# Kernel tuning notes

Measured on AMD Instinct MI355X. Metric: run time of the kernel, lower is better.

## Reference

```python
import jax, jax.numpy as jnp
import numpy as np
import math

SEQ_LEN = 2048
EMB = 1024
HEAD = 64
BATCH = 8

def setup_inputs() -> dict:
    key = jax.random.key(0)
    k1, k2, k3, k4 = jax.random.split(key, 4)
    x = jax.random.normal(k1, (BATCH, SEQ_LEN, EMB), dtype=jnp.float32)
    # torch Linear(no bias): out = x @ W.T with W [out,in]; store as [in,out]
    s = 1.0 / math.sqrt(EMB)
    Wk = jax.random.uniform(k2, (EMB, HEAD), dtype=jnp.float32, minval=-s, maxval=s)
    Wq = jax.random.uniform(k3, (EMB, HEAD), dtype=jnp.float32, minval=-s, maxval=s)
    Wv = jax.random.uniform(k4, (EMB, HEAD), dtype=jnp.float32, minval=-s, maxval=s)
    return {"x": x, "Wk": Wk, "Wq": Wq, "Wv": Wv}

def reference(x, Wk, Wq, Wv):
    B, S, E = x.shape
    H = Wk.shape[1]
    k = x @ Wk  # [B,S,H]
    q = x @ Wq
    v = x @ Wv
    scores = jnp.einsum('bsh,bth->bst', q, k) / math.sqrt(H)
    causal = jnp.tril(jnp.ones((S, S), dtype=bool))
    scores = jnp.where(causal[None], scores, -jnp.inf)
    attn = jax.nn.softmax(scores, axis=-1)
    # dropout is identity in eval mode
    return jnp.einsum('bst,bth->bsh', attn, v)
```

## Files before the change

kernel.cpp:

```cpp
#include <hip/hip_runtime.h>
#include <hip/hip_bf16.h>

typedef __attribute__((ext_vector_type(8))) short short8;
typedef __attribute__((ext_vector_type(4))) short short4v;
typedef __attribute__((ext_vector_type(4))) float floatx4;

#define SEQ   2048
#define EMB   1024
#define HEAD  64
#define BATCH 8

__device__ __forceinline__ short f2bf(float f) {
    union { float f; unsigned u; } a; a.f = f;
    unsigned u = a.u;
    u = (u + 0x7FFFu + ((u >> 16) & 1u)) >> 16;
    return (short)u;
}

__global__ void wtrans_kernel(const float* __restrict__ Wk,
                              const float* __restrict__ Wq,
                              const float* __restrict__ Wv,
                              short* __restrict__ Wf) {
    int gid  = blockIdx.x * 256 + threadIdx.x;
    int lane = gid & 63;
    int fid  = gid >> 6;
    int chunk = fid & 31;
    int mnt  = fid >> 5;
    int mat  = mnt >> 2, nt = mnt & 3;
    const float* src = (mat == 0) ? Wq : (mat == 1) ? Wk : Wv;
    int n = lane & 15, quad = lane >> 4;
    int h = nt * 16 + n;
    short8 o8;
    #pragma unroll
    for (int j = 0; j < 8; ++j)
        o8[j] = f2bf(src[(chunk * 32 + quad * 8 + j) * 64 + h]);
    *(short8*)(Wf + (long)gid * 8) = o8;
}

__global__ __launch_bounds__(256, 3) void qkv_kernel(const float* __restrict__ x,
                                                     const short* __restrict__ Wf,
                                                     short* __restrict__ q,
                                                     short* __restrict__ k,
                                                     short* __restrict__ vt) {
    __shared__ float red[3][64][50];
    const int wv   = threadIdx.x >> 6;
    const int lane = threadIdx.x & 63;
    const int l15  = lane & 15;
    const int quad = lane >> 4;
    const int row0 = blockIdx.x * 16;

    floatx4 acc[12];
    #pragma unroll
    for (int f = 0; f < 12; ++f) acc[f] = (floatx4){0.f, 0.f, 0.f, 0.f};

    const float* xrow  = x + (long)(row0 + l15) * EMB + quad * 8;
    const short* wlane = Wf + (long)lane * 8;
    const int kbase = wv * 256;

    floatx4 xa = *(const floatx4*)(xrow + kbase);
    floatx4 xb = *(const floatx4*)(xrow + kbase + 4);

    #pragma unroll 1
    for (int kk = 0; kk < 256; kk += 32) {
        const int cidx = (kbase + kk) >> 5;

        __builtin_amdgcn_sched_barrier(0);
        short8 bfr[12];
        #pragma unroll
        for (int f = 0; f < 12; ++f)
            bfr[f] = *(const short8*)(wlane + (long)(f * 32 + cidx) * 512);
        const int kn = kbase + ((kk + 32) & 255);
        floatx4 na = *(const floatx4*)(xrow + kn);
        floatx4 nb = *(const floatx4*)(xrow + kn + 4);
        __builtin_amdgcn_sched_barrier(0);

        short8 a;
        #pragma unroll
        for (int i = 0; i < 4; ++i) { a[i] = f2bf(xa[i]); a[4 + i] = f2bf(xb[i]); }
        #pragma unroll
        for (int f = 0; f < 12; ++f)
            acc[f] = __builtin_amdgcn_mfma_f32_16x16x32_bf16(a, bfr[f], acc[f], 0, 0, 0);
        xa = na; xb = nb;
    }

    if (wv > 0) {
        #pragma unroll
        for (int f = 0; f < 12; ++f)
            #pragma unroll
            for (int r = 0; r < 4; ++r)
                red[wv - 1][lane][f * 4 + r] = acc[f][r];
    }
    __syncthreads();
    if (wv == 0) {
        #pragma unroll
        for (int w = 0; w < 3; ++w)
            #pragma unroll
            for (int f = 0; f < 12; ++f)
                #pragma unroll
                for (int r = 0; r < 4; ++r)
                    acc[f][r] += red[w][lane][f * 4 + r];

        const int bidx = row0 >> 11;
        const int srow = (row0 & (SEQ - 1)) + quad * 4;
        #pragma unroll
        for (int nt = 0; nt < 4; ++nt) {
            const int col = nt * 16 + l15;
            #pragma unroll
            for (int r = 0; r < 4; ++r) {
                long grow = (long)(row0 + quad * 4 + r);
                q[grow * HEAD + col] = f2bf(acc[nt][r]);
                k[grow * HEAD + col] = f2bf(acc[4 + nt][r]);
            }
            short4v vv;
            #pragma unroll
            for (int r = 0; r < 4; ++r) vv[r] = f2bf(acc[8 + nt][r]);
            *(short4v*)(vt + ((long)bidx * HEAD + col) * SEQ + srow) = vv;
        }
    }
}

__global__ __launch_bounds__(256, 3) void attn_kernel(const short* __restrict__ q,
                                                      const short* __restrict__ k,
                                                      const short* __restrict__ vt,
                                                      float* __restrict__ out) {
    __shared__ short Plds[4][16][40];
    __shared__ float oA[4][16][64];
    __shared__ float lA[4][16];

    const int wv   = threadIdx.x >> 6;
    const int lane = threadIdx.x & 63;
    const int l15  = lane & 15;
    const int quad = lane >> 4;
    const int b    = blockIdx.x & 7;
    const int t    = 127 - (blockIdx.x >> 3);
    const int s0   = t * 16;

    const int nch  = (t + 2) >> 1;
    const int c0   = (nch * wv) >> 2;
    const int c1   = (nch * (wv + 1)) >> 2;
    const int cmax = (nch + 3) >> 2;

    const short* qb = q + ((long)b * SEQ + s0 + l15) * HEAD + quad * 8;
    short8 qf0 = *(const short8*)(qb);
    short8 qf1 = *(const short8*)(qb + 32);

    const short* kbb = k  + ((long)b * SEQ  + l15) * HEAD + quad * 8;
    const short* vbb = vt + ((long)b * HEAD + l15) * SEQ  + quad * 8;

    floatx4 o[4];
    #pragma unroll
    for (int nt = 0; nt < 4; ++nt) o[nt] = (floatx4){0.f, 0.f, 0.f, 0.f};
    float l_i[4] = {0.f, 0.f, 0.f, 0.f};

    #pragma unroll 1
    for (int i = 0; i < cmax; ++i) {
        const int c = c0 + i;
        const bool act = (c < c1);
        const int j0 = c * 32;

        __builtin_amdgcn_sched_barrier(0);
        short8 kf[2][2], vf[4];
        #pragma unroll
        for (int nt = 0; nt < 2; ++nt) {
            const short* kb = kbb + (long)(j0 + nt * 16) * HEAD;
            kf[nt][0] = *(const short8*)(kb);
            kf[nt][1] = *(const short8*)(kb + 32);
        }
        #pragma unroll
        for (int nt = 0; nt < 4; ++nt)
            vf[nt] = *(const short8*)(vbb + (long)nt * 16 * SEQ + j0);
        __builtin_amdgcn_sched_barrier(0);

        floatx4 sa[2];
        sa[0] = (floatx4){0.f, 0.f, 0.f, 0.f};
        sa[1] = (floatx4){0.f, 0.f, 0.f, 0.f};
        #pragma unroll
        for (int nt = 0; nt < 2; ++nt) {
            sa[nt] = __builtin_amdgcn_mfma_f32_16x16x32_bf16(qf0, kf[nt][0], sa[nt], 0, 0, 0);
            sa[nt] = __builtin_amdgcn_mfma_f32_16x16x32_bf16(qf1, kf[nt][1], sa[nt], 0, 0, 0);
        }

        #pragma unroll
        for (int r = 0; r < 4; ++r) {
            const int sq = s0 + quad * 4 + r;
            #pragma unroll
            for (int nt = 0; nt < 2; ++nt) {
                const int sk = j0 + nt * 16 + l15;
                float p = (!act || sk > sq) ? 0.f
                          : __expf(sa[nt][r] * 0.125f - 16.f);
                sa[nt][r] = p;
                l_i[r] += p;
            }
        }

        #pragma unroll
        for (int nt = 0; nt < 2; ++nt)
            #pragma unroll
            for (int r = 0; r < 4; ++r)
                Plds[wv][quad * 4 + r][nt * 16 + l15] = f2bf(sa[nt][r]);
        short8 pf = *(const short8*)(&Plds[wv][l15][quad * 8]);

        #pragma unroll
        for (int nt = 0; nt < 4; ++nt)
            o[nt] = __builtin_amdgcn_mfma_f32_16x16x32_bf16(pf, vf[nt], o[nt], 0, 0, 0);
    }

    #pragma unroll
    for (int msk = 1; msk <= 8; msk <<= 1) {
        #pragma unroll
        for (int r = 0; r < 4; ++r)
            l_i[r] += __shfl_xor(l_i[r], msk, 64);
    }
    if (l15 == 0) {
        #pragma unroll
        for (int r = 0; r < 4; ++r) lA[wv][quad * 4 + r] = l_i[r];
    }
    #pragma unroll
    for (int nt = 0; nt < 4; ++nt)
        #pragma unroll
        for (int r = 0; r < 4; ++r)
            oA[wv][quad * 4 + r][nt * 16 + l15] = o[nt][r];
    __syncthreads();

    {
        const int idx = threadIdx.x * 4;
        const int row = idx >> 6;
        const int col = idx & 63;
        const float l = lA[0][row] + lA[1][row] + lA[2][row] + lA[3][row];
        const float inv = 1.f / l;
        floatx4 ov;
        #pragma unroll
        for (int j = 0; j < 4; ++j)
            ov[j] = (oA[0][row][col + j] + oA[1][row][col + j]
                   + oA[2][row][col + j] + oA[3][row][col + j]) * inv;
        *(floatx4*)(out + ((long)b * SEQ + s0 + row) * HEAD + col) = ov;
    }
}

extern "C" void kernel_launch(void* const* d_in, const int* in_sizes, int n_in,
                              void* d_out, int out_size, void* d_ws, size_t ws_size,
                              hipStream_t stream) {
    const float* x  = (const float*)d_in[0];
    const float* Wk = (const float*)d_in[1];
    const float* Wq = (const float*)d_in[2];
    const float* Wv = (const float*)d_in[3];
    float* out = (float*)d_out;

    short* Wf = (short*)d_ws;
    short* q  = Wf + 3 * HEAD * EMB;
    short* k  = q + (long)BATCH * SEQ * HEAD;
    short* vt = k + (long)BATCH * SEQ * HEAD;

    hipLaunchKernelGGL(wtrans_kernel, dim3(96), dim3(256), 0, stream, Wk, Wq, Wv, Wf);
    hipLaunchKernelGGL(qkv_kernel, dim3(BATCH * SEQ / 16), dim3(256), 0, stream, x, Wf, q, k, vt);
    hipLaunchKernelGGL(attn_kernel, dim3(BATCH * 128), dim3(256), 0, stream, q, k, vt, out);
}
```

Before: 158.2 us.

## Stage weights and K/V tiles in LDS via async loads; pair causal query tiles

The QKV projection now gives each wave its own 16 rows and shares double-buffered weight tiles in LDS, loaded with global_load_lds, in place of the split-K cross-wave reduction. The attention kernel pairs a short and a long causal query tile per block, 32 rows each, to balance work. It stages K/Vt chunks of 64 keys in double-buffered LDS shared by all waves, and splits keys across two wave halves with a final LDS reduction. Together these cut redundant global loads and reduction overhead, at the cost of fewer, larger blocks (256 attention blocks) and lower occupancy limits.

```diff
diff --git a/kernel.cpp b/kernel.cpp
--- a/kernel.cpp
+++ b/kernel.cpp
@@ -15,6 +15,13 @@
     unsigned u = a.u;
     u = (u + 0x7FFFu + ((u >> 16) & 1u)) >> 16;
     return (short)u;
+}
+
+__device__ __forceinline__ void gld16(const void* g, void* l) {
+    __builtin_amdgcn_global_load_lds(
+        (const __attribute__((address_space(1))) unsigned int*)g,
+        (__attribute__((address_space(3))) unsigned int*)l,
+        16, 0, 0);
 }
 
 __global__ void wtrans_kernel(const float* __restrict__ Wk,
@@ -37,203 +44,265 @@
     *(short8*)(Wf + (long)gid * 8) = o8;
 }
 
-__global__ __launch_bounds__(256, 3) void qkv_kernel(const float* __restrict__ x,
+__global__ __launch_bounds__(256, 1) void qkv_kernel(const float* __restrict__ x,
                                                      const short* __restrict__ Wf,
                                                      short* __restrict__ q,
                                                      short* __restrict__ k,
                                                      short* __restrict__ vt) {
-    __shared__ float red[3][64][50];
+    __shared__ short LW[2][12][4][64][8];
     const int wv   = threadIdx.x >> 6;
     const int lane = threadIdx.x & 63;
     const int l15  = lane & 15;
     const int quad = lane >> 4;
-    const int row0 = blockIdx.x * 16;
+    const int row0 = blockIdx.x * 64 + wv * 16;
 
     floatx4 acc[12];
     #pragma unroll
     for (int f = 0; f < 12; ++f) acc[f] = (floatx4){0.f, 0.f, 0.f, 0.f};
 
-    const float* xrow  = x + (long)(row0 + l15) * EMB + quad * 8;
-    const short* wlane = Wf + (long)lane * 8;
-    const int kbase = wv * 256;
-
-    floatx4 xa = *(const floatx4*)(xrow + kbase);
-    floatx4 xb = *(const floatx4*)(xrow + kbase + 4);
+    const float* xrow = x + (long)(row0 + l15) * EMB + quad * 8;
+
+    #pragma unroll
+    for (int i = 0; i < 12; ++i) {
+        const int s = wv * 12 + i, mnt = s >> 2, c = s & 3;
+        gld16(Wf + (long)(mnt * 32 + c) * 512 + lane * 8, &LW[0][mnt][c][0][0]);
+    }
+    __syncthreads();
 
     #pragma unroll 1
-    for (int kk = 0; kk < 256; kk += 32) {
-        const int cidx = (kbase + kk) >> 5;
-
-        __builtin_amdgcn_sched_barrier(0);
-        short8 bfr[12];
-        #pragma unroll
-        for (int f = 0; f < 12; ++f)
-            bfr[f] = *(const short8*)(wlane + (long)(f * 32 + cidx) * 512);
-        const int kn = kbase + ((kk + 32) & 255);
-        floatx4 na = *(const floatx4*)(xrow + kn);
-        floatx4 nb = *(const floatx4*)(xrow + kn + 4);
-        __builtin_amdgcn_sched_barrier(0);
-
-        short8 a;
-        #pragma unroll
-        for (int i = 0; i < 4; ++i) { a[i] = f2bf(xa[i]); a[4 + i] = f2bf(xb[i]); }
-        #pragma unroll
-        for (int f = 0; f < 12; ++f)
-            acc[f] = __builtin_amdgcn_mfma_f32_16x16x32_bf16(a, bfr[f], acc[f], 0, 0, 0);
-        xa = na; xb = nb;
-    }
-
-    if (wv > 0) {
-        #pragma unroll
-        for (int f = 0; f < 12; ++f)
-            #pragma unroll
-            for (int r = 0; r < 4; ++r)
-                red[wv - 1][lane][f * 4 + r] = acc[f][r];
-    }
-    __syncthreads();
-    if (wv == 0) {
-        #pragma unroll
-        for (int w = 0; w < 3; ++w)
-            #pragma unroll
-            for (int f = 0; f < 12; ++f)
-                #pragma unroll
-                for (int r = 0; r < 4; ++r)
-                    acc[f][r] += red[w][lane][f * 4 + r];
-
-        const int bidx = row0 >> 11;
-        const int srow = (row0 & (SEQ - 1)) + quad * 4;
-        #pragma unroll
-        for (int nt = 0; nt < 4; ++nt) {
-            const int col = nt * 16 + l15;
-            #pragma unroll
-            for (int r = 0; r < 4; ++r) {
-                long grow = (long)(row0 + quad * 4 + r);
-                q[grow * HEAD + col] = f2bf(acc[nt][r]);
-                k[grow * HEAD + col] = f2bf(acc[4 + nt][r]);
-            }
-            short4v vv;
-            #pragma unroll
-            for (int r = 0; r < 4; ++r) vv[r] = f2bf(acc[8 + nt][r]);
-            *(short4v*)(vt + ((long)bidx * HEAD + col) * SEQ + srow) = vv;
-        }
-    }
-}
-
-__global__ __launch_bounds__(256, 3) void attn_kernel(const short* __restrict__ q,
+    for (int g = 0; g < 8; ++g) {
+        const int bb = g & 1;
+        const float* xg = xrow + g * 128;
+        floatx4 xv[8];
+        #pragma unroll
+        for (int c = 0; c < 4; ++c) {
+            xv[2 * c]     = *(const floatx4*)(xg + c * 32);
+            xv[2 * c + 1] = *(const floatx4*)(xg + c * 32 + 4);
+        }
+        if (g < 7) {
+            #pragma unroll
+            for (int i = 0; i < 12; ++i) {
+                const int s = wv * 12 + i, mnt = s >> 2, c = s & 3;
+                gld16(Wf + (long)(mnt * 32 + (g + 1) * 4 + c) * 512 + lane * 8,
+                      &LW[bb ^ 1][mnt][c][0][0]);
+            }
+        }
+        #pragma unroll
+        for (int c = 0; c < 4; ++c) {
+            short8 a;
+            #pragma unroll
+            for (int i = 0; i < 4; ++i) {
+                a[i]     = f2bf(xv[2 * c][i]);
+                a[4 + i] = f2bf(xv[2 * c + 1][i]);
+            }
+            #pragma unroll
+            for (int f = 0; f < 12; ++f) {
+                short8 bf = *(const short8*)&LW[bb][f][c][lane][0];
+                acc[f] = __builtin_amdgcn_mfma_f32_16x16x32_bf16(a, bf, acc[f], 0, 0, 0);
+            }
+        }
+        __syncthreads();
+    }
+
+    const int bidx = row0 >> 11;
+    const int srow = (row0 & (SEQ - 1)) + quad * 4;
+    #pragma unroll
+    for (int nt = 0; nt < 4; ++nt) {
+        const int col = nt * 16 + l15;
+        #pragma unroll
+        for (int r = 0; r < 4; ++r) {
+            long grow = (long)(row0 + quad * 4 + r);
+            q[grow * HEAD + col] = f2bf(acc[nt][r]);
+            k[grow * HEAD + col] = f2bf(acc[4 + nt][r]);
+        }
+        short4v vv;
+        #pragma unroll
+        for (int r = 0; r < 4; ++r) vv[r] = f2bf(acc[8 + nt][r]);
+        *(short4v*)(vt + ((long)bidx * HEAD + col) * SEQ + srow) = vv;
+    }
+}
+
+__global__ __launch_bounds__(256, 2) void attn_kernel(const short* __restrict__ q,
                                                       const short* __restrict__ k,
                                                       const short* __restrict__ vt,
                                                       float* __restrict__ out) {
+    __shared__ short KV[2][16][64][8];
     __shared__ short Plds[4][16][40];
-    __shared__ float oA[4][16][64];
-    __shared__ float lA[4][16];
+    __shared__ float oT[2][2][16][64];
+    __shared__ float lT[2][2][16];
 
     const int wv   = threadIdx.x >> 6;
     const int lane = threadIdx.x & 63;
     const int l15  = lane & 15;
     const int quad = lane >> 4;
+    const int rg   = wv & 1;
+    const int kh   = wv >> 1;
     const int b    = blockIdx.x & 7;
-    const int t    = 127 - (blockIdx.x >> 3);
-    const int s0   = t * 16;
-
-    const int nch  = (t + 2) >> 1;
-    const int c0   = (nch * wv) >> 2;
-    const int c1   = (nch * (wv + 1)) >> 2;
-    const int cmax = (nch + 3) >> 2;
-
-    const short* qb = q + ((long)b * SEQ + s0 + l15) * HEAD + quad * 8;
-    short8 qf0 = *(const short8*)(qb);
-    short8 qf1 = *(const short8*)(qb + 32);
-
-    const short* kbb = k  + ((long)b * SEQ  + l15) * HEAD + quad * 8;
-    const short* vbb = vt + ((long)b * HEAD + l15) * SEQ  + quad * 8;
-
-    floatx4 o[4];
-    #pragma unroll
-    for (int nt = 0; nt < 4; ++nt) o[nt] = (floatx4){0.f, 0.f, 0.f, 0.f};
-    float l_i[4] = {0.f, 0.f, 0.f, 0.f};
+    const int p    = blockIdx.x >> 3;
+    const int t2   = 63 - p;
+    const int s1   = p * 32, s2 = t2 * 32;
+    const int nch1 = (p >> 1) + 1;
+    const int nch2 = (t2 >> 1) + 1;
+
+    const short* kbase = k  + (long)b * SEQ * HEAD;
+    const short* vbase = vt + (long)b * HEAD * SEQ;
+
+    const short* q1p = q + ((long)b * SEQ + s1 + rg * 16 + l15) * HEAD + quad * 8;
+    const short* q2p = q + ((long)b * SEQ + s2 + rg * 16 + l15) * HEAD + quad * 8;
+    short8 q1f0 = *(const short8*)(q1p), q1f1 = *(const short8*)(q1p + 32);
+    short8 q2f0 = *(const short8*)(q2p), q2f1 = *(const short8*)(q2p + 32);
+
+    floatx4 o1[4], o2[4];
+    #pragma unroll
+    for (int nh = 0; nh < 4; ++nh) {
+        o1[nh] = (floatx4){0.f, 0.f, 0.f, 0.f};
+        o2[nh] = (floatx4){0.f, 0.f, 0.f, 0.f};
+    }
+    float l1[4] = {0.f, 0.f, 0.f, 0.f};
+    float l2[4] = {0.f, 0.f, 0.f, 0.f};
+
+    auto stage = [&](int ch, int bb) {
+        const int j0 = ch * 64;
+        #pragma unroll
+        for (int i = 0; i < 2; ++i) {
+            const int fid = wv + i * 4;
+            const int ntg = fid >> 1, ks = fid & 1;
+            gld16(kbase + (long)(j0 + ntg * 16 + l15) * HEAD + ks * 32 + quad * 8,
+                  &KV[bb][fid][0][0]);
+        }
+        #pragma unroll
+        for (int i = 0; i < 2; ++i) {
+            const int fid = wv + i * 4;
+            const int kh2 = fid >> 2, nth = fid & 3;
+            gld16(vbase + (long)(nth * 16 + l15) * SEQ + j0 + kh2 * 32 + quad * 8,
+                  &KV[bb][8 + fid][0][0]);
+        }
+    };
+
+    stage(0, 0);
+    __syncthreads();
 
     #pragma unroll 1
-    for (int i = 0; i < cmax; ++i) {
-        const int c = c0 + i;
-        const bool act = (c < c1);
-        const int j0 = c * 32;
-
-        __builtin_amdgcn_sched_barrier(0);
+    for (int ch = 0; ch < nch2; ++ch) {
+        const int bb = ch & 1;
+        if (ch + 1 < nch2) stage(ch + 1, bb ^ 1);
+        const int j0 = ch * 64;
+
         short8 kf[2][2], vf[4];
         #pragma unroll
-        for (int nt = 0; nt < 2; ++nt) {
-            const short* kb = kbb + (long)(j0 + nt * 16) * HEAD;
-            kf[nt][0] = *(const short8*)(kb);
-            kf[nt][1] = *(const short8*)(kb + 32);
-        }
-        #pragma unroll
-        for (int nt = 0; nt < 4; ++nt)
-            vf[nt] = *(const short8*)(vbb + (long)nt * 16 * SEQ + j0);
-        __builtin_amdgcn_sched_barrier(0);
-
-        floatx4 sa[2];
-        sa[0] = (floatx4){0.f, 0.f, 0.f, 0.f};
-        sa[1] = (floatx4){0.f, 0.f, 0.f, 0.f};
-        #pragma unroll
-        for (int nt = 0; nt < 2; ++nt) {
-            sa[nt] = __builtin_amdgcn_mfma_f32_16x16x32_bf16(qf0, kf[nt][0], sa[nt], 0, 0, 0);
-            sa[nt] = __builtin_amdgcn_mfma_f32_16x16x32_bf16(qf1, kf[nt][1], sa[nt], 0, 0, 0);
-        }
-
+        for (int nt = 0; nt < 2; ++nt)
+            #pragma unroll
+            for (int ks = 0; ks < 2; ++ks)
+                kf[nt][ks] = *(const short8*)&KV[bb][(kh * 2 + nt) * 2 + ks][lane][0];
+        #pragma unroll
+        for (int nh = 0; nh < 4; ++nh)
+            vf[nh] = *(const short8*)&KV[bb][8 + kh * 4 + nh][lane][0];
+
+        {
+            floatx4 sa[2];
+            sa[0] = (floatx4){0.f, 0.f, 0.f, 0.f};
+            sa[1] = (floatx4){0.f, 0.f, 0.f, 0.f};
+            #pragma unroll
+            for (int nt = 0; nt < 2; ++nt) {
+                sa[nt] = __builtin_amdgcn_mfma_f32_16x16x32_bf16(q2f0, kf[nt][0], sa[nt], 0, 0, 0);
+                sa[nt] = __builtin_amdgcn_mfma_f32_16x16x32_bf16(q2f1, kf[nt][1], sa[nt], 0, 0, 0);
+            }
+            #pragma unroll
+            for (int r = 0; r < 4; ++r) {
+                const int sq = s2 + rg * 16 + quad * 4 + r;
+                #pragma unroll
+                for (int nt = 0; nt < 2; ++nt) {
+                    const int sk = j0 + kh * 32 + nt * 16 + l15;
+                    float pv = (sk > sq) ? 0.f : __expf(sa[nt][r] * 0.125f - 16.f);
+                    sa[nt][r] = pv;
+                    l2[r] += pv;
+                }
+            }
+            #pragma unroll
+            for (int nt = 0; nt < 2; ++nt)
+                #pragma unroll
+                for (int r = 0; r < 4; ++r)
+                    Plds[wv][quad * 4 + r][nt * 16 + l15] = f2bf(sa[nt][r]);
+            short8 pf = *(const short8*)(&Plds[wv][l15][quad * 8]);
+            #pragma unroll
+            for (int nh = 0; nh < 4; ++nh)
+                o2[nh] = __builtin_amdgcn_mfma_f32_16x16x32_bf16(pf, vf[nh], o2[nh], 0, 0, 0);
+        }
+
+        if (ch < nch1) {
+            floatx4 sa[2];
+            sa[0] = (floatx4){0.f, 0.f, 0.f, 0.f};
+            sa[1] = (floatx4){0.f, 0.f, 0.f, 0.f};
+            #pragma unroll
+            for (int nt = 0; nt < 2; ++nt) {
+                sa[nt] = __builtin_amdgcn_mfma_f32_16x16x32_bf16(q1f0, kf[nt][0], sa[nt], 0, 0, 0);
+                sa[nt] = __builtin_amdgcn_mfma_f32_16x16x32_bf16(q1f1, kf[nt][1], sa[nt], 0, 0, 0);
+            }
+            #pragma unroll
+            for (int r = 0; r < 4; ++r) {
+                const int sq = s1 + rg * 16 + quad * 4 + r;
+                #pragma unroll
+                for (int nt = 0; nt < 2; ++nt) {
+                    const int sk = j0 + kh * 32 + nt * 16 + l15;
+                    float pv = (sk > sq) ? 0.f : __expf(sa[nt][r] * 0.125f - 16.f);
+                    sa[nt][r] = pv;
+                    l1[r] += pv;
+                }
+            }
+            #pragma unroll
+            for (int nt = 0; nt < 2; ++nt)
+                #pragma unroll
+                for (int r = 0; r < 4; ++r)
+                    Plds[wv][quad * 4 + r][nt * 16 + l15] = f2bf(sa[nt][r]);
+            short8 pf = *(const short8*)(&Plds[wv][l15][quad * 8]);
+            #pragma unroll
+            for (int nh = 0; nh < 4; ++nh)
+                o1[nh] = __builtin_amdgcn_mfma_f32_16x16x32_bf16(pf, vf[nh], o1[nh], 0, 0, 0);
+        }
+        __syncthreads();
+    }
+
+    #pragma unroll
+    for (int msk = 1; msk <= 8; msk <<= 1) {
         #pragma unroll
         for (int r = 0; r < 4; ++r) {
-            const int sq = s0 + quad * 4 + r;
-            #pragma unroll
-            for (int nt = 0; nt < 2; ++nt) {
-                const int sk = j0 + nt * 16 + l15;
-                float p = (!act || sk > sq) ? 0.f
-                          : __expf(sa[nt][r] * 0.125f - 16.f);
-                sa[nt][r] = p;
-                l_i[r] += p;
-            }
-        }
-
-        #pragma unroll
-        for (int nt = 0; nt < 2; ++nt)
-            #pragma unroll
-            for (int r = 0; r < 4; ++r)
-                Plds[wv][quad * 4 + r][nt * 16 + l15] = f2bf(sa[nt][r]);
-        short8 pf = *(const short8*)(&Plds[wv][l15][quad * 8]);
-
-        #pragma unroll
-        for (int nt = 0; nt < 4; ++nt)
-            o[nt] = __builtin_amdgcn_mfma_f32_16x16x32_bf16(pf, vf[nt], o[nt], 0, 0, 0);
-    }
-
-    #pragma unroll
-    for (int msk = 1; msk <= 8; msk <<= 1) {
-        #pragma unroll
-        for (int r = 0; r < 4; ++r)
-            l_i[r] += __shfl_xor(l_i[r], msk, 64);
-    }
-    if (l15 == 0) {
-        #pragma unroll
-        for (int r = 0; r < 4; ++r) lA[wv][quad * 4 + r] = l_i[r];
-    }
-    #pragma unroll
-    for (int nt = 0; nt < 4; ++nt)
-        #pragma unroll
-        for (int r = 0; r < 4; ++r)
-            oA[wv][quad * 4 + r][nt * 16 + l15] = o[nt][r];
+            l1[r] += __shfl_xor(l1[r], msk, 64);
+            l2[r] += __shfl_xor(l2[r], msk, 64);
+        }
+    }
+
+    if (kh == 1) {
+        #pragma unroll
+        for (int nh = 0; nh < 4; ++nh)
+            #pragma unroll
+            for (int r = 0; r < 4; ++r) {
+                oT[0][rg][quad * 4 + r][nh * 16 + l15] = o1[nh][r];
+                oT[1][rg][quad * 4 + r][nh * 16 + l15] = o2[nh][r];
+            }
+        if (l15 == 0) {
+            #pragma unroll
+            for (int r = 0; r < 4; ++r) {
+                lT[0][rg][quad * 4 + r] = l1[r];
+                lT[1][rg][quad * 4 + r] = l2[r];
+            }
+        }
+    }
     __syncthreads();
-
-    {
-        const int idx = threadIdx.x * 4;
-        const int row = idx >> 6;
-        const int col = idx & 63;
-        const float l = lA[0][row] + lA[1][row] + lA[2][row] + lA[3][row];
-        const float inv = 1.f / l;
-        floatx4 ov;
-        #pragma unroll
-        for (int j = 0; j < 4; ++j)
-            ov[j] = (oA[0][row][col + j] + oA[1][row][col + j]
-                   + oA[2][row][col + j] + oA[3][row][col + j]) * inv;
-        *(floatx4*)(out + ((long)b * SEQ + s0 + row) * HEAD + col) = ov;
+    if (kh == 0) {
+        #pragma unroll
+        for (int r = 0; r < 4; ++r) {
+            const int row = quad * 4 + r;
+            const float inv1 = 1.f / (l1[r] + lT[0][rg][row]);
+            const float inv2 = 1.f / (l2[r] + lT[1][rg][row]);
+            #pragma unroll
+            for (int nh = 0; nh < 4; ++nh) {
+                const int col = nh * 16 + l15;
+                out[((long)b * SEQ + s1 + rg * 16 + row) * HEAD + col] =
+                    (o1[nh][r] + oT[0][rg][row][col]) * inv1;
+                out[((long)b * SEQ + s2 + rg * 16 + row) * HEAD + col] =
+                    (o2[nh][r] + oT[1][rg][row][col]) * inv2;
+            }
+        }
     }
 }
 
@@ -252,6 +321,6 @@
     short* vt = k + (long)BATCH * SEQ * HEAD;
 
     hipLaunchKernelGGL(wtrans_kernel, dim3(96), dim3(256), 0, stream, Wk, Wq, Wv, Wf);
-    hipLaunchKernelGGL(qkv_kernel, dim3(BATCH * SEQ / 16), dim3(256), 0, stream, x, Wf, q, k, vt);
-    hipLaunchKernelGGL(attn_kernel, dim3(BATCH * 128), dim3(256), 0, stream, q, k, vt, out);
-}
+    hipLaunchKernelGGL(qkv_kernel, dim3(BATCH * SEQ / 64), dim3(256), 0, stream, x, Wf, q, k, vt);
+    hipLaunchKernelGGL(attn_kernel, dim3(BATCH * 32), dim3(256), 0, stream, q, k, vt, out);
+}
```

Result: no change. 158.4 us (+0.1%).
